# Optimization experiments

Measured on AMD Instinct MI355X. Metric: run time of the kernel, lower is better.

## Reference

```python
import jax, jax.numpy as jnp
import numpy as np
from jax import lax

EPROJS, DUNITS, ATT_DIM = 512, 1024, 320
ACONV_CHANS, ACONV_FILTS = 10, 100
B, T = 64, 2048
SCALING = 2.0


def setup_inputs() -> dict:
    key = jax.random.key(0)
    ks = jax.random.split(key, 10)
    enc_hs_pad = jax.random.normal(ks[0], (B, T, EPROJS), dtype=jnp.float32)
    # lengths in [T//2, T] so no row is fully masked
    enc_hs_len = jax.random.randint(ks[1], (B,), T // 2, T + 1).astype(jnp.int32)
    dec_z = jax.random.normal(ks[2], (B, DUNITS), dtype=jnp.float32)
    att_prev = jax.random.uniform(ks[3], (B, T), dtype=jnp.float32)
    # normalize att_prev like a prob. distribution over valid frames
    att_prev = att_prev / jnp.sum(att_prev, axis=1, keepdims=True)
    s = 0.02
    W_enc = jax.random.normal(ks[4], (ATT_DIM, EPROJS), dtype=jnp.float32) * s
    b_enc = jnp.zeros((ATT_DIM,), dtype=jnp.float32)
    W_dec = jax.random.normal(ks[5], (ATT_DIM, DUNITS), dtype=jnp.float32) * s
    W_att = jax.random.normal(ks[6], (ATT_DIM, ACONV_CHANS), dtype=jnp.float32) * s
    # Conv2d(1, aconv_chans, (1, 2*filts+1)) acts as 1D conv over time
    conv_w = jax.random.normal(ks[7], (ACONV_CHANS, 1, 2 * ACONV_FILTS + 1), dtype=jnp.float32) * s
    W_g = jax.random.normal(ks[8], (1, ATT_DIM), dtype=jnp.float32) * s
    b_g = jnp.zeros((1,), dtype=jnp.float32)
    return {
        "enc_hs_pad": enc_hs_pad, "enc_hs_len": enc_hs_len, "dec_z": dec_z,
        "att_prev": att_prev, "W_enc": W_enc, "b_enc": b_enc, "W_dec": W_dec,
        "W_att": W_att, "conv_w": conv_w, "W_g": W_g, "b_g": b_g,
    }


def reference(enc_hs_pad, enc_hs_len, dec_z, att_prev,
              W_enc, b_enc, W_dec, W_att, conv_w, W_g, b_g):
    # pre_compute_enc_h = mlp_enc(enc_h): [B, T, att_dim]
    pre_enc = jnp.einsum('bte,ae->bta', enc_hs_pad, W_enc) + b_enc
    # location conv: att_prev [B, T] -> [B, C, T] (SAME padding)
    att_conv = lax.conv_general_dilated(
        att_prev[:, None, :], conv_w, window_strides=(1,),
        padding=[(ACONV_FILTS, ACONV_FILTS)],
        dimension_numbers=('NCH', 'OIH', 'NCH'))
    # mlp_att over channels: [B, T, att_dim]
    att_feat = jnp.einsum('bct,ac->bta', att_conv, W_att)
    # mlp_dec(dec_z): [B, 1, att_dim]
    dec_feat = (dec_z @ W_dec.T)[:, None, :]
    # energies: gvec(tanh(sum)) -> [B, T]
    e = jnp.einsum('bta,a->bt', jnp.tanh(att_feat + pre_enc + dec_feat), W_g[0]) + b_g[0]
    # mask padded frames
    t_idx = jnp.arange(e.shape[1])
    pad_mask = t_idx[None, :] >= enc_hs_len[:, None]
    e = jnp.where(pad_mask, -jnp.inf, e)
    w = jax.nn.softmax(SCALING * e, axis=1)
    # context: weighted sum over encoder states -> [B, D_enc]
    c = jnp.einsum('bte,bt->be', enc_hs_pad, w)
    return (c, w)
```

## Files before the change

### kernel.cpp

```cpp
#include <hip/hip_runtime.h>
#include <hip/hip_bf16.h>

#define B_SZ 64
#define T_SZ 2048
#define EPROJS 512
#define DUNITS 1024
#define ATT_DIM 320
#define NCH 10
#define KFILT 201
#define PAD 100

typedef __attribute__((ext_vector_type(8))) __bf16 bf16x8;
typedef __attribute__((ext_vector_type(4))) float f32x4;
typedef __attribute__((ext_vector_type(8))) unsigned short u16x8;

__device__ __forceinline__ unsigned short f2b(float f) {
    __bf16 h = (__bf16)f;
    return __builtin_bit_cast(unsigned short, h);
}

__global__ void cvt_wenc(const float* __restrict__ W, unsigned short* __restrict__ out) {
    int i = (blockIdx.x * 256 + threadIdx.x) * 4;
    float4 v = *(const float4*)(W + i);
    ushort4 o;
    o.x = f2b(v.x); o.y = f2b(v.y); o.z = f2b(v.z); o.w = f2b(v.w);
    *(ushort4*)(out + i) = o;
}

__global__ void dec_feat_k(const float* __restrict__ dec_z, const float* __restrict__ W_dec,
                           const float* __restrict__ b_enc, float* __restrict__ df) {
    int b = blockIdx.x;
    int a = threadIdx.x;
    const float4* z = (const float4*)(dec_z + b * DUNITS);
    const float4* w = (const float4*)(W_dec + (size_t)a * DUNITS);
    float s = b_enc[a];
    #pragma unroll 4
    for (int d = 0; d < DUNITS / 4; ++d) {
        float4 zv = z[d], wv = w[d];
        s += zv.x * wv.x + zv.y * wv.y + zv.z * wv.z + zv.w * wv.w;
    }
    df[b * ATT_DIM + a] = s;
}

__global__ void conv_k(const float* __restrict__ ap, const float* __restrict__ cw,
                       float* __restrict__ out) {
    int b = blockIdx.x, c = blockIdx.y;
    __shared__ float s_ap[T_SZ];
    __shared__ float s_cw[KFILT];
    int tid = threadIdx.x;
    for (int i = tid; i < T_SZ; i += 256) s_ap[i] = ap[b * T_SZ + i];
    for (int i = tid; i < KFILT; i += 256) s_cw[i] = cw[c * KFILT + i];
    __syncthreads();
    for (int j = 0; j < T_SZ / 256; ++j) {
        int t = tid + j * 256;
        int klo = max(0, PAD - t);
        int khi = min(KFILT, T_SZ + PAD - t);
        float s = 0.f;
        for (int k = klo; k < khi; ++k) s += s_ap[t - PAD + k] * s_cw[k];
        out[((size_t)(b * NCH + c)) * T_SZ + t] = s;
    }
}

__global__ __launch_bounds__(512, 1) void energy_k(
    const float* __restrict__ enc, const unsigned short* __restrict__ wbf,
    const float* __restrict__ df, const float* __restrict__ att_conv,
    const float* __restrict__ W_att, const float* __restrict__ W_g,
    float* __restrict__ e_out)
{
    __shared__ unsigned short sW[ATT_DIM * 64];
    __shared__ float sDf[ATT_DIM], sWg[ATT_DIM], sWatt[ATT_DIM * NCH], sConv[NCH * 128];

    int tid = threadIdx.x;
    int lane = tid & 63, wave = tid >> 6;
    int blk = blockIdx.x;
    int b = blk >> 4;
    int t0 = (blk & 15) << 7;

    for (int i = tid; i < ATT_DIM; i += 512) { sDf[i] = df[b * ATT_DIM + i]; sWg[i] = W_g[i]; }
    for (int i = tid; i < ATT_DIM * NCH; i += 512) sWatt[i] = W_att[i];
    for (int i = tid; i < NCH * 128; i += 512)
        sConv[i] = att_conv[((size_t)(b * NCH + (i >> 7))) * T_SZ + t0 + (i & 127)];

    f32x4 acc[20];
    #pragma unroll
    for (int n = 0; n < 20; ++n) acc[n] = (f32x4){0.f, 0.f, 0.f, 0.f};

    int m15 = lane & 15, kg = lane >> 4;
    int row = t0 + wave * 16 + m15;
    const float* aP = enc + ((size_t)b * T_SZ + row) * EPROJS;

    for (int k0 = 0; k0 < EPROJS; k0 += 64) {
        __syncthreads();
        #pragma unroll
        for (int r = 0; r < 5; ++r) {
            int idx = r * 512 + tid;
            int wr = idx >> 3, k8 = idx & 7;
            u16x8 v = *(const u16x8*)(wbf + (size_t)wr * EPROJS + k0 + k8 * 8);
            int k8s = k8 ^ (wr & 7);
            *(u16x8*)(sW + wr * 64 + k8s * 8) = v;
        }
        __syncthreads();
        #pragma unroll
        for (int kk = 0; kk < 2; ++kk) {
            const float4 a0 = *(const float4*)(aP + k0 + kk * 32 + kg * 8);
            const float4 a1 = *(const float4*)(aP + k0 + kk * 32 + kg * 8 + 4);
            bf16x8 af;
            af[0] = (__bf16)a0.x; af[1] = (__bf16)a0.y; af[2] = (__bf16)a0.z; af[3] = (__bf16)a0.w;
            af[4] = (__bf16)a1.x; af[5] = (__bf16)a1.y; af[6] = (__bf16)a1.z; af[7] = (__bf16)a1.w;
            int k8r = kk * 4 + kg;
            #pragma unroll
            for (int nt = 0; nt < 20; ++nt) {
                int wr = nt * 16 + m15;
                bf16x8 wf = *(const bf16x8*)(sW + wr * 64 + ((k8r ^ (wr & 7)) * 8));
                acc[nt] = __builtin_amdgcn_mfma_f32_16x16x32_bf16(af, wf, acc[nt], 0, 0, 0);
            }
        }
    }

    int tl_base = wave * 16 + kg * 4;
    #pragma unroll
    for (int r = 0; r < 4; ++r) {
        int tl = tl_base + r;
        float s = 0.f;
        #pragma unroll
        for (int nt = 0; nt < 20; ++nt) {
            int col = nt * 16 + m15;
            float v = acc[nt][r] + sDf[col];
            float afeat = 0.f;
            #pragma unroll
            for (int c = 0; c < NCH; ++c) afeat += sWatt[col * NCH + c] * sConv[c * 128 + tl];
            v += afeat;
            v = fminf(fmaxf(v, -15.f), 15.f);
            float e2 = __expf(2.f * v);
            s += sWg[col] * ((e2 - 1.f) / (e2 + 1.f));
        }
        s += __shfl_xor(s, 1); s += __shfl_xor(s, 2);
        s += __shfl_xor(s, 4); s += __shfl_xor(s, 8);
        if (m15 == 0) e_out[b * T_SZ + t0 + tl] = s;
    }
}

__global__ void softmax_k(const float* __restrict__ e, const int* __restrict__ len,
                          float* __restrict__ w_out, float* __restrict__ w_ws) {
    int b = blockIdx.x, tid = threadIdx.x;
    int lane = tid & 63, wave = tid >> 6;
    int L = len[b];
    float ev[8];
    float m = -1e30f;
    #pragma unroll
    for (int i = 0; i < 8; ++i) {
        int t = tid + i * 256;
        float x = e[b * T_SZ + t];
        if (t >= L) x = -1e30f;
        ev[i] = x;
        m = fmaxf(m, x);
    }
    #pragma unroll
    for (int o = 32; o > 0; o >>= 1) m = fmaxf(m, __shfl_xor(m, o));
    __shared__ float sred[4];
    if (lane == 0) sred[wave] = m;
    __syncthreads();
    m = fmaxf(fmaxf(sred[0], sred[1]), fmaxf(sred[2], sred[3]));

    float ex[8];
    float sum = 0.f;
    #pragma unroll
    for (int i = 0; i < 8; ++i) { ex[i] = __expf(2.f * (ev[i] - m)); sum += ex[i]; }
    #pragma unroll
    for (int o = 32; o > 0; o >>= 1) sum += __shfl_xor(sum, o);
    __shared__ float sred2[4];
    if (lane == 0) sred2[wave] = sum;
    __syncthreads();
    sum = sred2[0] + sred2[1] + sred2[2] + sred2[3];
    float inv = 1.f / sum;
    #pragma unroll
    for (int i = 0; i < 8; ++i) {
        int t = tid + i * 256;
        float w = ex[i] * inv;
        w_out[b * T_SZ + t] = w;
        w_ws[b * T_SZ + t] = w;
    }
}

__global__ void ctx_partial_k(const float* __restrict__ enc, const float* __restrict__ w,
                              float* __restrict__ part) {
    int b = blockIdx.x, tc = blockIdx.y, tid = threadIdx.x;
    int half = tid >> 7;
    int c4 = tid & 127;
    f32x4 s = (f32x4){0.f, 0.f, 0.f, 0.f};
    int tb = tc * 128;
    #pragma unroll 4
    for (int i = half; i < 128; i += 2) {
        float wv = w[b * T_SZ + tb + i];
        f32x4 v = *(const f32x4*)(enc + ((size_t)b * T_SZ + tb + i) * EPROJS + c4 * 4);
        s += wv * v;
    }
    *(f32x4*)(part + ((size_t)(b * 32 + tc * 2 + half)) * EPROJS + c4 * 4) = s;
}

__global__ void ctx_reduce_k(const float* __restrict__ part, float* __restrict__ c_out) {
    int b = blockIdx.x;
    int c4 = threadIdx.x;
    f32x4 s = (f32x4){0.f, 0.f, 0.f, 0.f};
    #pragma unroll
    for (int tc = 0; tc < 32; ++tc)
        s += *(const f32x4*)(part + ((size_t)(b * 32 + tc)) * EPROJS + c4 * 4);
    *(f32x4*)(c_out + b * EPROJS + c4 * 4) = s;
}

extern "C" void kernel_launch(void* const* d_in, const int* in_sizes, int n_in,
                              void* d_out, int out_size, void* d_ws, size_t ws_size,
                              hipStream_t stream) {
    const float* enc      = (const float*)d_in[0];
    const int*   len      = (const int*)d_in[1];
    const float* dec_z    = (const float*)d_in[2];
    const float* att_prev = (const float*)d_in[3];
    const float* W_enc    = (const float*)d_in[4];
    const float* b_enc    = (const float*)d_in[5];
    const float* W_dec    = (const float*)d_in[6];
    const float* W_att    = (const float*)d_in[7];
    const float* conv_w   = (const float*)d_in[8];
    const float* W_g      = (const float*)d_in[9];

    char* ws = (char*)d_ws;
    size_t off = 0;
    unsigned short* wbf = (unsigned short*)(ws + off); off += (size_t)ATT_DIM * EPROJS * 2;
    float* e_buf  = (float*)(ws + off); off += (size_t)B_SZ * T_SZ * 4;
    float* dfb    = (float*)(ws + off); off += (size_t)B_SZ * ATT_DIM * 4;
    float* att_cv = (float*)(ws + off); off += (size_t)B_SZ * NCH * T_SZ * 4;
    float* w_ws   = (float*)(ws + off); off += (size_t)B_SZ * T_SZ * 4;
    float* part   = (float*)(ws + off); off += (size_t)B_SZ * 32 * EPROJS * 4;

    float* c_out = (float*)d_out;
    float* w_out = (float*)d_out + B_SZ * EPROJS;

    cvt_wenc<<<dim3(160), dim3(256), 0, stream>>>(W_enc, wbf);
    dec_feat_k<<<dim3(B_SZ), dim3(ATT_DIM), 0, stream>>>(dec_z, W_dec, b_enc, dfb);
    conv_k<<<dim3(B_SZ, NCH), dim3(256), 0, stream>>>(att_prev, conv_w, att_cv);
    energy_k<<<dim3(B_SZ * 16), dim3(512), 0, stream>>>(enc, wbf, dfb, att_cv, W_att, W_g, e_buf);
    softmax_k<<<dim3(B_SZ), dim3(256), 0, stream>>>(e_buf, len, w_out, w_ws);
    ctx_partial_k<<<dim3(B_SZ, 16), dim3(256), 0, stream>>>(enc, w_ws, part);
    ctx_reduce_k<<<dim3(B_SZ), dim3(128), 0, stream>>>(part, c_out);
}
```

Baseline: 250.6 us.

## Double-buffer W_enc tiles and prefetch encoder rows in energy kernel

Rewrites the energy kernel's K-loop to use a double-buffered LDS tile of 32 K-elements per step. The next tile of W_enc and the next encoder-row fragment are loaded into registers while MFMAs run on the current buffer, and only one barrier is issued per step. The LDS layout changes from an XOR-swizzled 64-wide tile to a kg-major layout, which may add bank conflicts. Separately, softmax no longer writes a duplicate copy of w to workspace, and the context kernel reads w_out directly.

```diff
diff --git a/kernel.cpp b/kernel.cpp
--- a/kernel.cpp
+++ b/kernel.cpp
@@ -67,14 +67,38 @@
     const float* __restrict__ W_att, const float* __restrict__ W_g,
     float* __restrict__ e_out)
 {
-    __shared__ unsigned short sW[ATT_DIM * 64];
+    __shared__ unsigned short sW[2][1280 * 8];
     __shared__ float sDf[ATT_DIM], sWg[ATT_DIM], sWatt[ATT_DIM * NCH], sConv[NCH * 128];
 
     int tid = threadIdx.x;
     int lane = tid & 63, wave = tid >> 6;
-    int blk = blockIdx.x;
-    int b = blk >> 4;
-    int t0 = (blk & 15) << 7;
+    int b = blockIdx.x >> 4;
+    int t0 = (blockIdx.x & 15) << 7;
+
+    int m15 = lane & 15, kg = lane >> 4;
+    int row = t0 + wave * 16 + m15;
+    const float* aP = enc + ((size_t)b * T_SZ + row) * EPROJS;
+
+    int q0 = tid >> 6;        int g0 = (q0 * 205) >> 10; int wr0 = tid - g0 * 320;
+    int i1 = tid + 512;  int q1 = i1 >> 6; int g1 = (q1 * 205) >> 10; int wr1 = i1 - g1 * 320;
+    int i2 = tid + 1024; int q2 = i2 >> 6; int g2 = (q2 * 205) >> 10; int wr2 = i2 - g2 * 320;
+    bool do2 = tid < 256;
+    const unsigned short* wp0 = wbf + (size_t)wr0 * EPROJS + g0 * 8;
+    const unsigned short* wp1 = wbf + (size_t)wr1 * EPROJS + g1 * 8;
+    const unsigned short* wp2 = wbf + (size_t)wr2 * EPROJS + g2 * 8;
+
+    {
+        u16x8 v0 = *(const u16x8*)wp0;
+        u16x8 v1 = *(const u16x8*)wp1;
+        *(u16x8*)(&sW[0][tid * 8]) = v0;
+        *(u16x8*)(&sW[0][i1 * 8]) = v1;
+        if (do2) {
+            u16x8 v2 = *(const u16x8*)wp2;
+            *(u16x8*)(&sW[0][i2 * 8]) = v2;
+        }
+    }
+    float4 a0 = *(const float4*)(aP + kg * 8);
+    float4 a1 = *(const float4*)(aP + kg * 8 + 4);
 
     for (int i = tid; i < ATT_DIM; i += 512) { sDf[i] = df[b * ATT_DIM + i]; sWg[i] = W_g[i]; }
     for (int i = tid; i < ATT_DIM * NCH; i += 512) sWatt[i] = W_att[i];
@@ -85,36 +109,37 @@
     #pragma unroll
     for (int n = 0; n < 20; ++n) acc[n] = (f32x4){0.f, 0.f, 0.f, 0.f};
 
-    int m15 = lane & 15, kg = lane >> 4;
-    int row = t0 + wave * 16 + m15;
-    const float* aP = enc + ((size_t)b * T_SZ + row) * EPROJS;
-
-    for (int k0 = 0; k0 < EPROJS; k0 += 64) {
-        __syncthreads();
+    __syncthreads();
+
+    for (int t = 0; t < 16; ++t) {
+        int cur = t & 1;
+        int kn = ((t + 1) & 15) * 32;
+        u16x8 w0 = *(const u16x8*)(wp0 + kn);
+        u16x8 w1 = *(const u16x8*)(wp1 + kn);
+        u16x8 w2;
+        if (do2) w2 = *(const u16x8*)(wp2 + kn);
+        float4 n0 = *(const float4*)(aP + kn + kg * 8);
+        float4 n1 = *(const float4*)(aP + kn + kg * 8 + 4);
+
+        bf16x8 af;
+        af[0] = (__bf16)a0.x; af[1] = (__bf16)a0.y; af[2] = (__bf16)a0.z; af[3] = (__bf16)a0.w;
+        af[4] = (__bf16)a1.x; af[5] = (__bf16)a1.y; af[6] = (__bf16)a1.z; af[7] = (__bf16)a1.w;
+        const unsigned short* sw = sW[cur];
         #pragma unroll
-        for (int r = 0; r < 5; ++r) {
-            int idx = r * 512 + tid;
-            int wr = idx >> 3, k8 = idx & 7;
-            u16x8 v = *(const u16x8*)(wbf + (size_t)wr * EPROJS + k0 + k8 * 8);
-            int k8s = k8 ^ (wr & 7);
-            *(u16x8*)(sW + wr * 64 + k8s * 8) = v;
+        for (int nt = 0; nt < 20; ++nt) {
+            int wr = nt * 16 + m15;
+            bf16x8 wf = *(const bf16x8*)(sw + (kg * 320 + wr) * 8);
+            acc[nt] = __builtin_amdgcn_mfma_f32_16x16x32_bf16(af, wf, acc[nt], 0, 0, 0);
         }
-        __syncthreads();
-        #pragma unroll
-        for (int kk = 0; kk < 2; ++kk) {
-            const float4 a0 = *(const float4*)(aP + k0 + kk * 32 + kg * 8);
-            const float4 a1 = *(const float4*)(aP + k0 + kk * 32 + kg * 8 + 4);
-            bf16x8 af;
-            af[0] = (__bf16)a0.x; af[1] = (__bf16)a0.y; af[2] = (__bf16)a0.z; af[3] = (__bf16)a0.w;
-            af[4] = (__bf16)a1.x; af[5] = (__bf16)a1.y; af[6] = (__bf16)a1.z; af[7] = (__bf16)a1.w;
-            int k8r = kk * 4 + kg;
-            #pragma unroll
-            for (int nt = 0; nt < 20; ++nt) {
-                int wr = nt * 16 + m15;
-                bf16x8 wf = *(const bf16x8*)(sW + wr * 64 + ((k8r ^ (wr & 7)) * 8));
-                acc[nt] = __builtin_amdgcn_mfma_f32_16x16x32_bf16(af, wf, acc[nt], 0, 0, 0);
-            }
-        }
+
+        unsigned short* swn = (unsigned short*)sW[cur ^ 1];
+        *(u16x8*)(&swn[tid * 8]) = w0;
+        *(u16x8*)(&swn[i1 * 8]) = w1;
+        if (do2) *(u16x8*)(&swn[i2 * 8]) = w2;
+        a0 = n0; a1 = n1;
+
+        asm volatile("s_waitcnt lgkmcnt(0)" ::: "memory");
+        __builtin_amdgcn_s_barrier();
     }
 
     int tl_base = wave * 16 + kg * 4;
@@ -141,7 +166,7 @@
 }
 
 __global__ void softmax_k(const float* __restrict__ e, const int* __restrict__ len,
-                          float* __restrict__ w_out, float* __restrict__ w_ws) {
+                          float* __restrict__ w_out) {
     int b = blockIdx.x, tid = threadIdx.x;
     int lane = tid & 63, wave = tid >> 6;
     int L = len[b];
@@ -176,9 +201,7 @@
     #pragma unroll
     for (int i = 0; i < 8; ++i) {
         int t = tid + i * 256;
-        float w = ex[i] * inv;
-        w_out[b * T_SZ + t] = w;
-        w_ws[b * T_SZ + t] = w;
+        w_out[b * T_SZ + t] = ex[i] * inv;
     }
 }
 
@@ -228,7 +251,6 @@
     float* e_buf  = (float*)(ws + off); off += (size_t)B_SZ * T_SZ * 4;
     float* dfb    = (float*)(ws + off); off += (size_t)B_SZ * ATT_DIM * 4;
     float* att_cv = (float*)(ws + off); off += (size_t)B_SZ * NCH * T_SZ * 4;
-    float* w_ws   = (float*)(ws + off); off += (size_t)B_SZ * T_SZ * 4;
     float* part   = (float*)(ws + off); off += (size_t)B_SZ * 32 * EPROJS * 4;
 
     float* c_out = (float*)d_out;
@@ -238,7 +260,7 @@
     dec_feat_k<<<dim3(B_SZ), dim3(ATT_DIM), 0, stream>>>(dec_z, W_dec, b_enc, dfb);
     conv_k<<<dim3(B_SZ, NCH), dim3(256), 0, stream>>>(att_prev, conv_w, att_cv);
     energy_k<<<dim3(B_SZ * 16), dim3(512), 0, stream>>>(enc, wbf, dfb, att_cv, W_att, W_g, e_buf);
-    softmax_k<<<dim3(B_SZ), dim3(256), 0, stream>>>(e_buf, len, w_out, w_ws);
-    ctx_partial_k<<<dim3(B_SZ, 16), dim3(256), 0, stream>>>(enc, w_ws, part);
+    softmax_k<<<dim3(B_SZ), dim3(256), 0, stream>>>(e_buf, len, w_out);
+    ctx_partial_k<<<dim3(B_SZ, 16), dim3(256), 0, stream>>>(enc, w_out, part);
     ctx_reduce_k<<<dim3(B_SZ), dim3(128), 0, stream>>>(part, c_out);
 }
```

Result: no change. 251.8 us (+0.5%).
